# Kernel optimization log

Hardware: AMD Instinct MI355X
Metric: run time of the kernel (lower is better)

## Reference

```python
import jax, jax.numpy as jnp
import numpy as np
from functools import partial

IMG = 1024           # input image H = W
H_OUT = W_OUT = 64   # backbone feature map
SCALES = (64.0, 128.0, 256.0, 512.0)
RATIOS = (0.5, 1.0, 2.0)
A = len(SCALES) * len(RATIOS)          # 12 anchors per location
N_ANC = H_OUT * W_OUT * A              # 49152
PRENMS = 12000                          # hard-coded prenms_topn in source
TOP_N = 256
NMS_THRESH = 0.7
NEG = jnp.float32(-1e9)


def make_anchors():
    """Anchors in xyxy, grid order (h, w, anchor) to match permute(0,2,3,1).reshape."""
    stride_h = IMG / H_OUT
    stride_w = IMG / W_OUT
    cy = (np.arange(H_OUT, dtype=np.float32) + 0.5) * stride_h   # [H]
    cx = (np.arange(W_OUT, dtype=np.float32) + 0.5) * stride_w   # [W]
    ws, hs = [], []
    for s in SCALES:
        for r in RATIOS:
            ws.append(s * np.sqrt(r))
            hs.append(s / np.sqrt(r))
    ws = np.asarray(ws, np.float32)  # [A]
    hs = np.asarray(hs, np.float32)
    cy_g = cy[:, None, None]
    cx_g = cx[None, :, None]
    x1 = cx_g - ws / 2
    y1 = cy_g - hs / 2
    x2 = cx_g + ws / 2
    y2 = cy_g + hs / 2
    anc = np.stack(np.broadcast_arrays(x1, y1, x2, y2), axis=-1)  # [H,W,A,4]
    return jnp.asarray(anc.reshape(-1, 4))


def delta_to_boxes(deltas, anchors):
    """Standard R-CNN decoding. deltas [B,N,4], anchors [N,4] xyxy -> boxes xyxy."""
    wa = anchors[:, 2] - anchors[:, 0]
    ha = anchors[:, 3] - anchors[:, 1]
    cxa = anchors[:, 0] + 0.5 * wa
    cya = anchors[:, 1] + 0.5 * ha
    cx = deltas[..., 0] * wa + cxa
    cy = deltas[..., 1] * ha + cya
    w = wa * jnp.exp(deltas[..., 2])
    h = ha * jnp.exp(deltas[..., 3])
    return jnp.stack([cx - 0.5 * w, cy - 0.5 * h, cx + 0.5 * w, cy + 0.5 * h], axis=-1)


def iou_one_vs_all(box, boxes):
    x1 = jnp.maximum(box[0], boxes[:, 0])
    y1 = jnp.maximum(box[1], boxes[:, 1])
    x2 = jnp.minimum(box[2], boxes[:, 2])
    y2 = jnp.minimum(box[3], boxes[:, 3])
    inter = jnp.clip(x2 - x1, 0) * jnp.clip(y2 - y1, 0)
    area_a = (box[2] - box[0]) * (box[3] - box[1])
    area_b = (boxes[:, 2] - boxes[:, 0]) * (boxes[:, 3] - boxes[:, 1])
    return inter / (area_a + area_b - inter + 1e-7)


def nms_one(boxes, scores):
    """Greedy NMS, fixed TOP_N iterations. boxes [P,4], scores [P] -> [TOP_N,4]."""
    def body(i, carry):
        sel, sc = carry
        j = jnp.argmax(sc)
        best = boxes[j]
        valid = sc[j] > NEG * 0.5
        ious = iou_one_vs_all(best, boxes)
        sc = jnp.where(ious > NMS_THRESH, NEG, sc)  # also suppresses `best` itself
        sel = sel.at[i].set(jnp.where(valid, best, jnp.zeros(4, boxes.dtype)))
        return sel, sc
    sel0 = jnp.zeros((TOP_N, 4), boxes.dtype)
    sel, _ = jax.lax.fori_loop(0, TOP_N, body, (sel0, scores))
    return sel


def setup_inputs() -> dict:
    key = jax.random.key(0)
    ks = jax.random.split(key, 7)
    B, C, HID = 16, 512, 512
    return {
        "features": jax.random.normal(ks[0], (B, C, H_OUT, W_OUT), jnp.float32),
        "conv_w": jax.random.normal(ks[1], (HID, C, 3, 3), jnp.float32) * 0.01,
        "conv_b": jnp.zeros((HID,), jnp.float32),
        "reg_w": jax.random.normal(ks[2], (A * 4, HID), jnp.float32) * 0.01,
        "reg_b": jnp.zeros((A * 4,), jnp.float32),
        "conf_w": jax.random.normal(ks[3], (A, HID), jnp.float32) * 0.01,
        "conf_b": jnp.zeros((A,), jnp.float32),
    }


def reference(features, conv_w, conv_b, reg_w, reg_b, conf_w, conf_b):
    B = features.shape[0]
    anchors = make_anchors()                                   # [N,4]
    # proposal head: Conv3x3 -> (dropout=identity at inference) -> ReLU
    h = jax.lax.conv_general_dilated(
        features, conv_w, window_strides=(1, 1), padding="SAME",
        dimension_numbers=("NCHW", "OIHW", "NCHW"))
    h = jax.nn.relu(h + conv_b[None, :, None, None])            # [B,HID,H,W]
    # 1x1 heads, then permute(0,2,3,1).reshape as in source
    reg = jnp.einsum("bchw,oc->bhwo", h, reg_w) + reg_b         # [B,H,W,A*4]
    reg = reg.reshape(B, -1, 4)                                 # [B,N,4]
    conf = jnp.einsum("bchw,oc->bhwo", h, conf_w) + conf_b      # [B,H,W,A]
    conf = conf.reshape(B, -1)                                  # [B,N]

    boxes = delta_to_boxes(reg, anchors)                        # [B,N,4]
    top_conf, top_idx = jax.lax.top_k(conf, PRENMS)             # [B,P]
    top_boxes = jnp.take_along_axis(boxes, top_idx[..., None], axis=1)
    # clip boxes to image
    top_boxes = jnp.clip(top_boxes, 0.0, float(IMG))
    # size mask (degenerate boxes) -> kill score instead of filtering
    w = top_boxes[..., 2] - top_boxes[..., 0]
    hh = top_boxes[..., 3] - top_boxes[..., 1]
    top_conf = jnp.where((w >= 1.0) & (hh >= 1.0), top_conf, NEG)
    proposals = jax.vmap(nms_one)(top_boxes, top_conf)          # [B,TOP_N,4]
    return proposals
```

## Files before the change

kernel.cpp:

```cpp
#include <hip/hip_runtime.h>
#include <math.h>

#define NEGD (-1000000000.0)

typedef __attribute__((ext_vector_type(4))) double d4;

__global__ void make_wT(const float* __restrict__ reg_w,
                        const float* __restrict__ conf_w,
                        double* __restrict__ wT)
{
    int i = blockIdx.x * 256 + threadIdx.x;
    if (i >= 512 * 64) return;
    int c = i >> 6, o = i & 63;
    double v = 0.0;
    if (o < 48)      v = (double)reg_w[o * 512 + c];
    else if (o < 60) v = (double)conf_w[(o - 48) * 512 + c];
    wT[i] = v;
}

__global__ __launch_bounds__(512, 4) void conv3x3_mfma_f64(
    const float* __restrict__ f, const float* __restrict__ w,
    const float* __restrict__ bias, double* __restrict__ h, int b0)
{
    __shared__ double Xs[8 * 198];
    __shared__ double Ws[64 * 73];
    const int bl   = blockIdx.z;
    const int b    = b0 + bl;
    const int oc0  = blockIdx.y * 64;
    const int y    = blockIdx.x;
    const int tid  = threadIdx.x;
    const int wv   = tid >> 6;
    const int lane = tid & 63;
    const int fk   = lane >> 4;
    const int fm   = lane & 15;
    const int ocw  = (wv & 3) * 16;
    const int x0   = (wv >> 2) * 32;

    d4 zz = {0.0, 0.0, 0.0, 0.0};
    d4 p1 = __builtin_amdgcn_mfma_f64_16x16x4f64((double)fm, 1.0, zz, 0, 0, 0);
    d4 p2 = __builtin_amdgcn_mfma_f64_16x16x4f64(1.0, (double)fm, zz, 0, 0, 0);
    int ocl[4], pxl[4];
#pragma unroll
    for (int r = 0; r < 4; ++r) {
        ocl[r] = (int)(p1[r] * 0.25);
        pxl[r] = (int)(p2[r] * 0.25);
    }

    d4 acc0 = {0.0, 0.0, 0.0, 0.0};
    d4 acc1 = {0.0, 0.0, 0.0, 0.0};

    for (int ic0 = 0; ic0 < 512; ic0 += 8) {
        for (int e = tid; e < 1584; e += 512) {
            int ic = e / 198, r = e - ic * 198;
            int ry = r / 66, cx = r - ry * 66;
            int gy = y + ry - 1, gx = cx - 1;
            double v = 0.0;
            if ((unsigned)gy < 64u && (unsigned)gx < 64u)
                v = (double)f[((b * 512 + ic0 + ic) * 64 + gy) * 64 + gx];
            Xs[e] = v;
        }
        for (int e = tid; e < 4608; e += 512) {
            int oc = e / 72, it = e - oc * 72;
            Ws[oc * 73 + it] = (double)w[(oc0 + oc) * 4608 + ic0 * 9 + it];
        }
        __syncthreads();

#pragma unroll
        for (int s = 0; s < 2; ++s) {
            const int ick = s * 4 + fk;
            const double* xb = &Xs[ick * 198 + x0 + fm];
            const double* wb = &Ws[(ocw + fm) * 73 + ick * 9];
#pragma unroll
            for (int ky = 0; ky < 3; ++ky) {
#pragma unroll
                for (int kx = 0; kx < 3; ++kx) {
                    double av  = wb[ky * 3 + kx];
                    double b0v = xb[ky * 66 + kx];
                    double b1v = xb[ky * 66 + kx + 16];
                    acc0 = __builtin_amdgcn_mfma_f64_16x16x4f64(av, b0v, acc0, 0, 0, 0);
                    acc1 = __builtin_amdgcn_mfma_f64_16x16x4f64(av, b1v, acc1, 0, 0, 0);
                }
            }
        }
        __syncthreads();
    }

#pragma unroll
    for (int r = 0; r < 4; ++r) {
        int oc = oc0 + ocw + ocl[r];
        double bz = (double)bias[oc];
        double v0 = acc0[r] + bz; v0 = v0 > 0.0 ? v0 : 0.0;
        double v1 = acc1[r] + bz; v1 = v1 > 0.0 ? v1 : 0.0;
        double* hp = &h[(((long)bl * 512 + oc) * 64 + y) * 64];
        hp[x0 + pxl[r]]      = v0;
        hp[x0 + pxl[r] + 16] = v1;
    }
}

__global__ __launch_bounds__(256) void head_gemm_f64(
    const double* __restrict__ h, const double* __restrict__ wT,
    const float* __restrict__ reg_b, const float* __restrict__ conf_b,
    double* __restrict__ rc, int b0)
{
    __shared__ double h_t[32 * 128];
    __shared__ double w_t[32 * 64];
    const int bl  = blockIdx.y;
    const int b   = b0 + bl;
    const int hw0 = blockIdx.x * 128;
    const int tid = threadIdx.x;
    const int to  = tid >> 4;
    const int tp  = tid & 15;

    double acc[8][4];
#pragma unroll
    for (int j = 0; j < 8; ++j)
#pragma unroll
        for (int k = 0; k < 4; ++k) acc[j][k] = 0.0;

    for (int c0 = 0; c0 < 512; c0 += 32) {
        for (int e = tid; e < 32 * 128; e += 256) {
            int c = e >> 7, p = e & 127;
            h_t[e] = h[(bl * 512 + c0 + c) * 4096 + hw0 + p];
        }
        for (int e = tid; e < 32 * 64; e += 256) {
            w_t[e] = wT[(c0 + (e >> 6)) * 64 + (e & 63)];
        }
        __syncthreads();
#pragma unroll 4
        for (int c = 0; c < 32; ++c) {
            double wa[4], hv[8];
#pragma unroll
            for (int k = 0; k < 4; ++k) wa[k] = w_t[c * 64 + to * 4 + k];
#pragma unroll
            for (int j = 0; j < 8; ++j) hv[j] = h_t[c * 128 + tp * 8 + j];
#pragma unroll
            for (int j = 0; j < 8; ++j)
#pragma unroll
                for (int k = 0; k < 4; ++k)
                    acc[j][k] = fma(hv[j], wa[k], acc[j][k]);
        }
        __syncthreads();
    }
#pragma unroll
    for (int k = 0; k < 4; ++k) {
        int o = to * 4 + k;
        double bz = (o < 48) ? (double)reg_b[o] : (o < 60 ? (double)conf_b[o - 48] : 0.0);
#pragma unroll
        for (int j = 0; j < 8; ++j) acc[j][k] += bz;
    }
#pragma unroll
    for (int j = 0; j < 8; ++j)
#pragma unroll
        for (int k = 0; k < 4; ++k)
            rc[(long)(b * 4096 + hw0 + tp * 8 + j) * 64 + to * 4 + k] = acc[j][k];
}

__global__ void decode_f64(const double* __restrict__ rc,
                           double* __restrict__ boxes,
                           double* __restrict__ craw,
                           double* __restrict__ nsc)
{
    int g = blockIdx.x * 256 + threadIdx.x;
    if (g >= 16 * 49152) return;
    int b = g / 49152, n = g - b * 49152;
    int hw = n / 12, a = n - hw * 12;
    int y = hw >> 6, x = hw & 63;
    int si = a / 3, ri = a - si * 3;

    double s  = (double)(64 << si);
    double sr = (ri == 0) ? 0.70710678118654752440
              : (ri == 1) ? 1.0 : 1.41421356237309504880;
    float aw = (float)(s * sr);
    float ah = (float)(s / sr);

    float cyc = ((float)y + 0.5f) * 16.f;
    float cxc = ((float)x + 0.5f) * 16.f;
    float ax1 = cxc - aw * 0.5f;
    float ay1 = cyc - ah * 0.5f;
    float ax2 = cxc + aw * 0.5f;
    float ay2 = cyc + ah * 0.5f;

    double wa  = (double)ax2 - (double)ax1;
    double ha  = (double)ay2 - (double)ay1;
    double cxa = (double)ax1 + 0.5 * wa;
    double cya = (double)ay1 + 0.5 * ha;

    const double* r = rc + (long)(b * 4096 + hw) * 64;
    double d0 = r[a * 4 + 0];
    double d1 = r[a * 4 + 1];
    double d2 = r[a * 4 + 2];
    double d3 = r[a * 4 + 3];
    double conf = r[48 + a];

    double pcx = d0 * wa + cxa;
    double pcy = d1 * ha + cya;
    double pw  = wa * exp(d2);
    double ph  = ha * exp(d3);

    double bx1 = pcx - 0.5 * pw;
    double by1 = pcy - 0.5 * ph;
    double bx2 = pcx + 0.5 * pw;
    double by2 = pcy + 0.5 * ph;

    bx1 = fmin(fmax(bx1, 0.0), 1024.0);
    by1 = fmin(fmax(by1, 0.0), 1024.0);
    bx2 = fmin(fmax(bx2, 0.0), 1024.0);
    by2 = fmin(fmax(by2, 0.0), 1024.0);

    double ww = bx2 - bx1, hh = by2 - by1;
    bool valid = (ww >= 1.0) && (hh >= 1.0);

    double* bo = boxes + (long)g * 4;
    bo[0] = bx1; bo[1] = by1; bo[2] = bx2; bo[3] = by2;
    craw[g] = conf;
    nsc[g]  = valid ? conf : NEGD;
}

__device__ __forceinline__ unsigned long long fkey64(double d) {
    unsigned long long u = (unsigned long long)__double_as_longlong(d);
    return (u & 0x8000000000000000ull) ? ~u : (u | 0x8000000000000000ull);
}

__global__ __launch_bounds__(1024) void topk_thresh64(
    const double* __restrict__ craw, unsigned long long* __restrict__ tinfo)
{
    __shared__ unsigned hist[256];
    __shared__ unsigned long long s_prefix;
    __shared__ int s_k;
    const int b = blockIdx.x, tid = threadIdx.x;
    const double* cb = craw + b * 49152;
    unsigned long long prefix = 0; int k = 12000;
    for (int pass = 0; pass < 8; ++pass) {
        const int shift = 56 - 8 * pass;
        if (tid < 256) hist[tid] = 0;
        __syncthreads();
        for (int i = tid; i < 49152; i += 1024) {
            unsigned long long u = fkey64(cb[i]);
            bool ok = (pass == 0) ||
                      ((u >> (shift + 8)) == (prefix >> (shift + 8)));
            if (ok) atomicAdd(&hist[(unsigned)(u >> shift) & 255u], 1u);
        }
        __syncthreads();
        if (tid == 0) {
            int kk = k, d = 0;
            for (int dd = 255; dd >= 0; --dd) {
                int c = (int)hist[dd];
                if (kk <= c) { d = dd; break; }
                kk -= c;
            }
            s_prefix = prefix | ((unsigned long long)d << shift);
            s_k = kk;
        }
        __syncthreads();
        prefix = s_prefix; k = s_k;
        __syncthreads();
    }
    if (tid == 0) { tinfo[b * 2] = prefix; tinfo[b * 2 + 1] = (unsigned long long)k; }
}

__global__ __launch_bounds__(1024) void compact_topk64(
    const double* __restrict__ craw, const double* __restrict__ boxes,
    const double* __restrict__ nsc, const unsigned long long* __restrict__ tinfo,
    double* __restrict__ cbox, double* __restrict__ csc)
{
    const int b = blockIdx.x, tid = threadIdx.x;
    const unsigned long long T = tinfo[b * 2];
    const unsigned E = (unsigned)tinfo[b * 2 + 1];
    const double* cb = craw + b * 49152;
    const int i0 = tid * 48;

    unsigned gt = 0, eq = 0;
    for (int j = 0; j < 48; ++j) {
        unsigned long long u = fkey64(cb[i0 + j]);
        gt += (u > T); eq += (u == T);
    }
    unsigned gi = gt, ei = eq;
    for (int d = 1; d < 64; d <<= 1) {
        unsigned g2 = __shfl_up(gi, d), e2 = __shfl_up(ei, d);
        if ((tid & 63) >= d) { gi += g2; ei += e2; }
    }
    __shared__ unsigned wg[16], we[16];
    if ((tid & 63) == 63) { wg[tid >> 6] = gi; we[tid >> 6] = ei; }
    __syncthreads();
    if (tid < 16) {
        unsigned a = wg[tid], c = we[tid];
        for (int d = 1; d < 16; d <<= 1) {
            unsigned a2 = __shfl_up(a, d), c2 = __shfl_up(c, d);
            if (tid >= d) { a += a2; c += c2; }
        }
        wg[tid] = a; we[tid] = c;
    }
    __syncthreads();
    unsigned g = gi - gt + ((tid >> 6) ? wg[(tid >> 6) - 1] : 0u);
    unsigned e = ei - eq + ((tid >> 6) ? we[(tid >> 6) - 1] : 0u);

    double* ob = cbox + (long)b * 12000 * 4;
    double* os = csc  + b * 12000;
    const double* bb = boxes + (long)b * 49152 * 4;
    const double* ns = nsc + b * 49152;
    for (int j = 0; j < 48; ++j) {
        int idx = i0 + j;
        unsigned long long u = fkey64(cb[idx]);
        if (u > T) {
            unsigned pos = g + (e < E ? e : E);
            ob[pos * 4 + 0] = bb[(long)idx * 4 + 0];
            ob[pos * 4 + 1] = bb[(long)idx * 4 + 1];
            ob[pos * 4 + 2] = bb[(long)idx * 4 + 2];
            ob[pos * 4 + 3] = bb[(long)idx * 4 + 3];
            os[pos] = ns[idx];
            ++g;
        } else if (u == T) {
            if (e < E) {
                unsigned pos = g + e;
                ob[pos * 4 + 0] = bb[(long)idx * 4 + 0];
                ob[pos * 4 + 1] = bb[(long)idx * 4 + 1];
                ob[pos * 4 + 2] = bb[(long)idx * 4 + 2];
                ob[pos * 4 + 3] = bb[(long)idx * 4 + 3];
                os[pos] = ns[idx];
            }
            ++e;
        }
    }
}

__global__ __launch_bounds__(1024) void nms64(
    const double* __restrict__ cbox, const double* __restrict__ csc,
    float* __restrict__ out)
{
    const int b = blockIdx.x, tid = threadIdx.x;
    const double* B4 = cbox + (long)b * 12000 * 4;
    const double* S  = csc  + b * 12000;

    double sc[12];
#pragma unroll
    for (int j = 0; j < 12; ++j) {
        int idx = tid + 1024 * j;
        sc[j] = (idx < 12000) ? S[idx] : NEGD;
    }

    __shared__ double wvv[16];
    __shared__ int    wii[16];
    float* O = out + b * 1024;

    for (int it = 0; it < 256; ++it) {
        double bv = sc[0]; int bj = 0;
#pragma unroll
        for (int j = 1; j < 12; ++j)
            if (sc[j] > bv) { bv = sc[j]; bj = j; }
        int bidx = tid + 1024 * bj;
        for (int d = 1; d < 64; d <<= 1) {
            double ov = __shfl_xor(bv, d);
            int    oi = __shfl_xor(bidx, d);
            if (ov > bv || (ov == bv && oi < bidx)) { bv = ov; bidx = oi; }
        }
        if ((tid & 63) == 0) { wvv[tid >> 6] = bv; wii[tid >> 6] = bidx; }
        __syncthreads();
        if (tid == 0) {
            double v = wvv[0]; int ix = wii[0];
            for (int q = 1; q < 16; ++q)
                if (wvv[q] > v || (wvv[q] == v && wii[q] < ix)) { v = wvv[q]; ix = wii[q]; }
            wvv[0] = v; wii[0] = ix;
        }
        __syncthreads();
        double bestv = wvv[0];
        int    besti = wii[0];
        const double* bb = B4 + (long)besti * 4;
        double b0 = bb[0], b1 = bb[1], b2 = bb[2], b3 = bb[3];
        bool valid = bestv > -5.0e8;
        if (tid == 0) {
            O[it * 4 + 0] = valid ? (float)b0 : 0.f;
            O[it * 4 + 1] = valid ? (float)b1 : 0.f;
            O[it * 4 + 2] = valid ? (float)b2 : 0.f;
            O[it * 4 + 3] = valid ? (float)b3 : 0.f;
        }
        double areaA = (b2 - b0) * (b3 - b1);
#pragma unroll
        for (int j = 0; j < 12; ++j) {
            if (sc[j] > -5.0e8) {
                int idx = tid + 1024 * j;
                const double* pb = B4 + (long)idx * 4;
                double x1 = fmax(b0, pb[0]);
                double y1 = fmax(b1, pb[1]);
                double x2 = fmin(b2, pb[2]);
                double y2 = fmin(b3, pb[3]);
                double iw = x2 - x1; iw = iw > 0.0 ? iw : 0.0;
                double ih = y2 - y1; ih = ih > 0.0 ? ih : 0.0;
                double inter = iw * ih;
                double areaB = (pb[2] - pb[0]) * (pb[3] - pb[1]);
                if (inter > 0.7 * (areaA + areaB - inter + 1e-7)) sc[j] = NEGD;
            }
        }
        __syncthreads();
    }
}

extern "C" void kernel_launch(void* const* d_in, const int* in_sizes, int n_in,
                              void* d_out, int out_size, void* d_ws, size_t ws_size,
                              hipStream_t stream)
{
    const float* f      = (const float*)d_in[0];
    const float* conv_w = (const float*)d_in[1];
    const float* conv_b = (const float*)d_in[2];
    const float* reg_w  = (const float*)d_in[3];
    const float* reg_b  = (const float*)d_in[4];
    const float* conf_w = (const float*)d_in[5];
    const float* conf_b = (const float*)d_in[6];

    double* ws = (double*)d_ws;
    double* wT    = ws;
    double* h     = ws + 32768;
    double* rc    = ws + 8421376;
    double* boxes = ws + 12615680;
    double* craw  = ws + 15761408;
    double* nsc   = ws + 16547840;
    double* cbox  = ws + 17334272;
    double* csc   = ws + 18102272;
    unsigned long long* tinfo = (unsigned long long*)(ws + 18294272);

    hipLaunchKernelGGL(make_wT, dim3(128), dim3(256), 0, stream, reg_w, conf_w, wT);
    for (int q = 0; q < 4; ++q) {
        int b0 = q * 4;
        hipLaunchKernelGGL(conv3x3_mfma_f64, dim3(64, 8, 4), dim3(512), 0, stream,
                           f, conv_w, conv_b, h, b0);
        hipLaunchKernelGGL(head_gemm_f64, dim3(32, 4), dim3(256), 0, stream,
                           h, wT, reg_b, conf_b, rc, b0);
    }
    hipLaunchKernelGGL(decode_f64, dim3(3072), dim3(256), 0, stream,
                       rc, boxes, craw, nsc);
    hipLaunchKernelGGL(topk_thresh64, dim3(16), dim3(1024), 0, stream, craw, tinfo);
    hipLaunchKernelGGL(compact_topk64, dim3(16), dim3(1024), 0, stream,
                       craw, boxes, nsc, tinfo, cbox, csc);
    hipLaunchKernelGGL(nms64, dim3(16), dim3(1024), 0, stream,
                       cbox, csc, (float*)d_out);
}
```

Before: 9.194 ms.

## Retile f64 conv into 32oc x 2-row blocks with 2x2 MFMA register tiles

```diff
diff --git a/kernel.cpp b/kernel.cpp
--- a/kernel.cpp
+++ b/kernel.cpp
@@ -4,6 +4,13 @@
 #define NEGD (-1000000000.0)
 
 typedef __attribute__((ext_vector_type(4))) double d4;
+typedef __attribute__((ext_vector_type(2))) double d2;
+
+__global__ void convert_w64(const float* __restrict__ w, double* __restrict__ w64)
+{
+    int i = blockIdx.x * 1024 + threadIdx.x;
+    if (i < 2359296) w64[i] = (double)w[i];
+}
 
 __global__ void make_wT(const float* __restrict__ reg_w,
                         const float* __restrict__ conf_w,
@@ -18,23 +25,23 @@
     wT[i] = v;
 }
 
-__global__ __launch_bounds__(512, 4) void conv3x3_mfma_f64(
-    const float* __restrict__ f, const float* __restrict__ w,
+__global__ __launch_bounds__(256, 4) void conv3x3_mfma_f64(
+    const float* __restrict__ f, const double* __restrict__ w64,
     const float* __restrict__ bias, double* __restrict__ h, int b0)
 {
-    __shared__ double Xs[8 * 198];
-    __shared__ double Ws[64 * 73];
+    __shared__ double Xs[8 * 264];
+    __shared__ double Ws[32 * 74];
     const int bl   = blockIdx.z;
     const int b    = b0 + bl;
-    const int oc0  = blockIdx.y * 64;
-    const int y    = blockIdx.x;
+    const int oc0  = blockIdx.y * 32;
+    const int y0   = blockIdx.x * 2;
     const int tid  = threadIdx.x;
     const int wv   = tid >> 6;
     const int lane = tid & 63;
     const int fk   = lane >> 4;
     const int fm   = lane & 15;
-    const int ocw  = (wv & 3) * 16;
-    const int x0   = (wv >> 2) * 32;
+    const int ryo  = wv >> 1;
+    const int xb0  = (wv & 1) * 32;
 
     d4 zz = {0.0, 0.0, 0.0, 0.0};
     d4 p1 = __builtin_amdgcn_mfma_f64_16x16x4f64((double)fm, 1.0, zz, 0, 0, 0);
@@ -46,54 +53,67 @@
         pxl[r] = (int)(p2[r] * 0.25);
     }
 
-    d4 acc0 = {0.0, 0.0, 0.0, 0.0};
-    d4 acc1 = {0.0, 0.0, 0.0, 0.0};
+    d4 a00 = zz, a01 = zz, a10 = zz, a11 = zz;
 
     for (int ic0 = 0; ic0 < 512; ic0 += 8) {
-        for (int e = tid; e < 1584; e += 512) {
-            int ic = e / 198, r = e - ic * 198;
+        for (int e = tid; e < 2112; e += 256) {
+            int ic = e / 264, r = e - ic * 264;
             int ry = r / 66, cx = r - ry * 66;
-            int gy = y + ry - 1, gx = cx - 1;
+            int gy = y0 + ry - 1, gx = cx - 1;
             double v = 0.0;
             if ((unsigned)gy < 64u && (unsigned)gx < 64u)
                 v = (double)f[((b * 512 + ic0 + ic) * 64 + gy) * 64 + gx];
             Xs[e] = v;
         }
-        for (int e = tid; e < 4608; e += 512) {
-            int oc = e / 72, it = e - oc * 72;
-            Ws[oc * 73 + it] = (double)w[(oc0 + oc) * 4608 + ic0 * 9 + it];
+        for (int e = tid; e < 1152; e += 256) {
+            int oc = e / 36, jj = (e - oc * 36) * 2;
+            d2 v = *(const d2*)&w64[(size_t)(oc0 + oc) * 4608 + ic0 * 9 + jj];
+            *(d2*)&Ws[oc * 74 + jj] = v;
         }
         __syncthreads();
 
 #pragma unroll
         for (int s = 0; s < 2; ++s) {
             const int ick = s * 4 + fk;
-            const double* xb = &Xs[ick * 198 + x0 + fm];
-            const double* wb = &Ws[(ocw + fm) * 73 + ick * 9];
+            const double* xr  = &Xs[ick * 264 + ryo * 66 + xb0 + fm];
+            const double* wr0 = &Ws[fm * 74 + ick * 9];
+            const double* wr1 = &Ws[(fm + 16) * 74 + ick * 9];
 #pragma unroll
             for (int ky = 0; ky < 3; ++ky) {
 #pragma unroll
                 for (int kx = 0; kx < 3; ++kx) {
-                    double av  = wb[ky * 3 + kx];
-                    double b0v = xb[ky * 66 + kx];
-                    double b1v = xb[ky * 66 + kx + 16];
-                    acc0 = __builtin_amdgcn_mfma_f64_16x16x4f64(av, b0v, acc0, 0, 0, 0);
-                    acc1 = __builtin_amdgcn_mfma_f64_16x16x4f64(av, b1v, acc1, 0, 0, 0);
+                    double a0v = wr0[ky * 3 + kx];
+                    double a1v = wr1[ky * 3 + kx];
+                    double b0v = xr[ky * 66 + kx];
+                    double b1v = xr[ky * 66 + kx + 16];
+                    a00 = __builtin_amdgcn_mfma_f64_16x16x4f64(a0v, b0v, a00, 0, 0, 0);
+                    a01 = __builtin_amdgcn_mfma_f64_16x16x4f64(a0v, b1v, a01, 0, 0, 0);
+                    a10 = __builtin_amdgcn_mfma_f64_16x16x4f64(a1v, b0v, a10, 0, 0, 0);
+                    a11 = __builtin_amdgcn_mfma_f64_16x16x4f64(a1v, b1v, a11, 0, 0, 0);
                 }
             }
         }
         __syncthreads();
     }
 
+    const int y = y0 + ryo;
 #pragma unroll
     for (int r = 0; r < 4; ++r) {
-        int oc = oc0 + ocw + ocl[r];
-        double bz = (double)bias[oc];
-        double v0 = acc0[r] + bz; v0 = v0 > 0.0 ? v0 : 0.0;
-        double v1 = acc1[r] + bz; v1 = v1 > 0.0 ? v1 : 0.0;
-        double* hp = &h[(((long)bl * 512 + oc) * 64 + y) * 64];
-        hp[x0 + pxl[r]]      = v0;
-        hp[x0 + pxl[r] + 16] = v1;
+        int ocA = oc0 + ocl[r];
+        int ocB = oc0 + 16 + ocl[r];
+        int px0 = xb0 + pxl[r];
+        double bzA = (double)bias[ocA];
+        double bzB = (double)bias[ocB];
+        double v00 = a00[r] + bzA; v00 = v00 > 0.0 ? v00 : 0.0;
+        double v01 = a01[r] + bzA; v01 = v01 > 0.0 ? v01 : 0.0;
+        double v10 = a10[r] + bzB; v10 = v10 > 0.0 ? v10 : 0.0;
+        double v11 = a11[r] + bzB; v11 = v11 > 0.0 ? v11 : 0.0;
+        double* hA = &h[(((long)bl * 512 + ocA) * 64 + y) * 64];
+        double* hB = &h[(((long)bl * 512 + ocB) * 64 + y) * 64];
+        hA[px0]      = v00;
+        hA[px0 + 16] = v01;
+        hB[px0]      = v10;
+        hB[px0 + 16] = v11;
     }
 }
 
@@ -188,13 +208,13 @@
     const double* r = rc + (long)(b * 4096 + hw) * 64;
     double d0 = r[a * 4 + 0];
     double d1 = r[a * 4 + 1];
-    double d2 = r[a * 4 + 2];
+    double d2v = r[a * 4 + 2];
     double d3 = r[a * 4 + 3];
     double conf = r[48 + a];
 
     double pcx = d0 * wa + cxa;
     double pcy = d1 * ha + cya;
-    double pw  = wa * exp(d2);
+    double pw  = wa * exp(d2v);
     double ph  = ha * exp(d3);
 
     double bx1 = pcx - 0.5 * pw;
@@ -416,12 +436,14 @@
     double* cbox  = ws + 17334272;
     double* csc   = ws + 18102272;
     unsigned long long* tinfo = (unsigned long long*)(ws + 18294272);
-
+    double* w64   = boxes;
+
+    hipLaunchKernelGGL(convert_w64, dim3(2304), dim3(1024), 0, stream, conv_w, w64);
     hipLaunchKernelGGL(make_wT, dim3(128), dim3(256), 0, stream, reg_w, conf_w, wT);
     for (int q = 0; q < 4; ++q) {
         int b0 = q * 4;
-        hipLaunchKernelGGL(conv3x3_mfma_f64, dim3(64, 8, 4), dim3(512), 0, stream,
-                           f, conv_w, conv_b, h, b0);
+        hipLaunchKernelGGL(conv3x3_mfma_f64, dim3(32, 16, 4), dim3(256), 0, stream,
+                           f, w64, conv_b, h, b0);
         hipLaunchKernelGGL(head_gemm_f64, dim3(32, 4), dim3(256), 0, stream,
                            h, wT, reg_b, conf_b, rc, b0);
     }
```

After: 8.490 ms. 7.7% less time.
